# Kernel optimization log

Measured on AMD Instinct MI355X. Metric: run time of the kernel, lower is better.

Reference implementation:

```python
import jax, jax.numpy as jnp
import numpy as np

LN_EPS = 1e-5

def layernorm(x, g, b):
    mu = jnp.mean(x, axis=-1, keepdims=True)
    var = jnp.mean(jnp.square(x - mu), axis=-1, keepdims=True)
    return (x - mu) * jax.lax.rsqrt(var + LN_EPS) * g + b

def setup_inputs() -> dict:
    B, T, C, H = 4, 1024, 1024, 16
    hd = C // H
    key = jax.random.key(0)
    ks = jax.random.split(key, 16)
    s = 0.02
    inp = {
        "x":  jax.random.normal(ks[0], (B, T, C), jnp.float32),
        # per-head QKV projections, stacked over heads: [H, C, hd] / [H, hd]
        "Wq": jax.random.normal(ks[1], (H, C, hd), jnp.float32) * s,
        "bq": jax.random.normal(ks[2], (H, hd), jnp.float32) * s,
        "Wk": jax.random.normal(ks[3], (H, C, hd), jnp.float32) * s,
        "bk": jax.random.normal(ks[4], (H, hd), jnp.float32) * s,
        "Wv": jax.random.normal(ks[5], (H, C, hd), jnp.float32) * s,
        "bv": jax.random.normal(ks[6], (H, hd), jnp.float32) * s,
        # LayerNorm params: ln1, ln2 (decoder), lnf (inside FeedForward)
        "g1": 1.0 + jax.random.normal(ks[7], (C,), jnp.float32) * s,
        "b1": jax.random.normal(ks[8], (C,), jnp.float32) * s,
        "g2": 1.0 + jax.random.normal(ks[9], (C,), jnp.float32) * s,
        "b2": jax.random.normal(ks[10], (C,), jnp.float32) * s,
        "gf": 1.0 + jax.random.normal(ks[11], (C,), jnp.float32) * s,
        "bf": jax.random.normal(ks[12], (C,), jnp.float32) * s,
        # FFN
        "W1": jax.random.normal(ks[13], (C, 4 * C), jnp.float32) * s,
        "b1f": jnp.zeros((4 * C,), jnp.float32),
        "W2": jax.random.normal(ks[14], (4 * C, C), jnp.float32) * s,
        "b2f": jnp.zeros((C,), jnp.float32),
    }
    return inp

def reference(x, Wq, bq, Wk, bk, Wv, bv, g1, b1, g2, b2, gf, bf, W1, b1f, W2, b2f):
    B, T, C = x.shape
    h = layernorm(x, g1, b1)                      # ln1
    # multi-head causal attention (per-head projections stacked on H)
    q = jnp.einsum("btc,hcd->bhtd", h, Wq) + bq[None, :, None, :]
    k = jnp.einsum("btc,hcd->bhtd", h, Wk) + bk[None, :, None, :]
    v = jnp.einsum("btc,hcd->bhtd", h, Wv) + bv[None, :, None, :]
    # NOTE: original scales by C**-0.5 (n_embd), not head_size**-0.5
    att = jnp.einsum("bhtd,bhsd->bhts", q, k) / jnp.sqrt(jnp.float32(C))
    causal = jnp.tril(jnp.ones((T, T), bool))
    att = jnp.where(causal, att, -jnp.inf)
    att = jax.nn.softmax(att, axis=-1)
    o = jnp.einsum("bhts,bhsd->bhtd", att, v)     # [B,H,T,hd]
    o = jnp.transpose(o, (0, 2, 1, 3)).reshape(B, T, C)  # concat heads
    x2 = h + o
    x3 = layernorm(x2, g2, b2)                    # ln2
    # FeedForward: hf = ln(x3); out = net(hf) + hf  (residual uses post-LN!)
    hf = layernorm(x3, gf, bf)
    ff = jax.nn.relu(hf @ W1 + b1f) @ W2 + b2f + hf
    return x3 + ff                                # dropout is identity in eval
```

## Files before the change

### kernel.cpp

```cpp
#include <hip/hip_runtime.h>
#include <hip/hip_bf16.h>


typedef __attribute__((ext_vector_type(8))) short short8;
typedef __attribute__((ext_vector_type(4))) short short4v;
typedef __attribute__((ext_vector_type(4))) float f32x4;

#define DEVI static __device__ __forceinline__

#define BAR() __builtin_amdgcn_s_barrier()
#define SB0() __builtin_amdgcn_sched_barrier(0)
#define LGKM0()                                         \
  {                                                     \
    asm volatile("s_waitcnt lgkmcnt(0)" ::: "memory");  \
    __builtin_amdgcn_sched_barrier(0);                  \
  }
#define VMW(n)                                              \
  {                                                         \
    asm volatile("s_waitcnt vmcnt(" #n ")" ::: "memory");   \
    __builtin_amdgcn_sched_barrier(0);                      \
  }

DEVI void gload_lds16(const void* g, void* l) {
  __builtin_amdgcn_global_load_lds(
      (const __attribute__((address_space(1))) void*)g,
      (__attribute__((address_space(3))) void*)l, 16, 0, 0);
}

DEVI float bf2f(short s) {
  union { float f; unsigned u; } cv;
  cv.u = ((unsigned)(unsigned short)s) << 16;
  return cv.f;
}
DEVI short f2bf(float f) {
  union { float f; unsigned u; } cv;
  cv.f = f;
  unsigned u = cv.u;
  u += 0x7FFFu + ((u >> 16) & 1u);
  return (short)(u >> 16);
}

DEVI void block_reduce2(float& s, float& s2, float* red, int t) {
#pragma unroll
  for (int off = 1; off < 64; off <<= 1) {
    s += __shfl_xor(s, off, 64);
    s2 += __shfl_xor(s2, off, 64);
  }
  __syncthreads();
  if ((t & 63) == 0) { red[(t >> 6) * 2] = s; red[(t >> 6) * 2 + 1] = s2; }
  __syncthreads();
  s = red[0] + red[2] + red[4] + red[6];
  s2 = red[1] + red[3] + red[5] + red[7];
}

DEVI void xcd_swz(int gx, int gy, int& bx, int& by) {
  const int flat = blockIdx.y * gx + blockIdx.x;
  const int c = (gx * gy) >> 3;
  const int nf = (flat & 7) * c + (flat >> 3);
  bx = nf % gx;
  by = nf / gx;
}

__global__ __launch_bounds__(256) void transpose_to_bf16(
    const float* __restrict__ in, short* __restrict__ out, int R, int C) {
  __shared__ float tile[32][33];
  const int b = blockIdx.z;
  in += (size_t)b * R * C;
  out += (size_t)b * R * C;
  const int r0 = blockIdx.y * 32, c0 = blockIdx.x * 32;
  const int tx = threadIdx.x, ty = threadIdx.y;
#pragma unroll
  for (int i = 0; i < 32; i += 8)
    tile[ty + i][tx] = in[(size_t)(r0 + ty + i) * C + c0 + tx];
  __syncthreads();
#pragma unroll
  for (int i = 0; i < 32; i += 8)
    out[(size_t)(c0 + ty + i) * R + r0 + tx] = f2bf(tile[tx][ty + i]);
}

__global__ __launch_bounds__(256) void transpose_qkv(
    const float* __restrict__ Wq, const float* __restrict__ Wk,
    const float* __restrict__ Wv, short* __restrict__ out) {
  __shared__ float tile[32][33];
  const int z = blockIdx.z;
  const int sel = z >> 4, b = z & 15;
  const float* in = (sel == 0) ? Wq : (sel == 1) ? Wk : Wv;
  in += (size_t)b * 1024 * 64;
  short* o = out + (size_t)sel * 1024 * 1024 + (size_t)b * 1024 * 64;
  const int r0 = blockIdx.y * 32, c0 = blockIdx.x * 32;
  const int tx = threadIdx.x, ty = threadIdx.y;
#pragma unroll
  for (int i = 0; i < 32; i += 8)
    tile[ty + i][tx] = in[(size_t)(r0 + ty + i) * 64 + c0 + tx];
  __syncthreads();
#pragma unroll
  for (int i = 0; i < 32; i += 8)
    o[(size_t)(c0 + ty + i) * 1024 + r0 + tx] = f2bf(tile[tx][ty + i]);
}

__global__ __launch_bounds__(256) void ln1_kernel(
    const float* __restrict__ x, const float* __restrict__ g,
    const float* __restrict__ b, short* __restrict__ hb) {
  __shared__ float red[8];
  const int row = blockIdx.x, t = threadIdx.x;
  float4 v = ((const float4*)(x + (size_t)row * 1024))[t];
  float s = v.x + v.y + v.z + v.w;
  float s2 = v.x * v.x + v.y * v.y + v.z * v.z + v.w * v.w;
  block_reduce2(s, s2, red, t);
  const float mu = s * (1.0f / 1024.0f);
  const float rstd = rsqrtf(s2 * (1.0f / 1024.0f) - mu * mu + 1e-5f);
  float4 gv = ((const float4*)g)[t], bv = ((const float4*)b)[t];
  short4v p = {f2bf((v.x - mu) * rstd * gv.x + bv.x),
               f2bf((v.y - mu) * rstd * gv.y + bv.y),
               f2bf((v.z - mu) * rstd * gv.z + bv.z),
               f2bf((v.w - mu) * rstd * gv.w + bv.w)};
  ((short4v*)(hb + (size_t)row * 1024))[t] = p;
}

__global__ __launch_bounds__(256) void ln2f_kernel(
    const short* __restrict__ hbb, const short* __restrict__ ob,
    const float* __restrict__ g2, const float* __restrict__ b2,
    const float* __restrict__ gf, const float* __restrict__ bfp,
    short* __restrict__ x3, short* __restrict__ hfb) {
  __shared__ float red[8];
  const int row = blockIdx.x, t = threadIdx.x;
  short4v hv4 = ((const short4v*)(hbb + (size_t)row * 1024))[t];
  short4v ov4 = ((const short4v*)(ob + (size_t)row * 1024))[t];
  float4 v;
  v.x = bf2f(hv4.x) + bf2f(ov4.x);
  v.y = bf2f(hv4.y) + bf2f(ov4.y);
  v.z = bf2f(hv4.z) + bf2f(ov4.z);
  v.w = bf2f(hv4.w) + bf2f(ov4.w);
  float s = v.x + v.y + v.z + v.w;
  float s2 = v.x * v.x + v.y * v.y + v.z * v.z + v.w * v.w;
  block_reduce2(s, s2, red, t);
  float mu = s * (1.0f / 1024.0f);
  float rstd = rsqrtf(s2 * (1.0f / 1024.0f) - mu * mu + 1e-5f);
  float4 gv = ((const float4*)g2)[t], bv = ((const float4*)b2)[t];
  float4 xv;
  xv.x = (v.x - mu) * rstd * gv.x + bv.x;
  xv.y = (v.y - mu) * rstd * gv.y + bv.y;
  xv.z = (v.z - mu) * rstd * gv.z + bv.z;
  xv.w = (v.w - mu) * rstd * gv.w + bv.w;
  short4v xp = {f2bf(xv.x), f2bf(xv.y), f2bf(xv.z), f2bf(xv.w)};
  ((short4v*)(x3 + (size_t)row * 1024))[t] = xp;
  s = xv.x + xv.y + xv.z + xv.w;
  s2 = xv.x * xv.x + xv.y * xv.y + xv.z * xv.z + xv.w * xv.w;
  block_reduce2(s, s2, red, t);
  mu = s * (1.0f / 1024.0f);
  rstd = rsqrtf(s2 * (1.0f / 1024.0f) - mu * mu + 1e-5f);
  float4 gv2 = ((const float4*)gf)[t], bv2 = ((const float4*)bfp)[t];
  short4v pk = {f2bf((xv.x - mu) * rstd * gv2.x + bv2.x),
                f2bf((xv.y - mu) * rstd * gv2.y + bv2.y),
                f2bf((xv.z - mu) * rstd * gv2.z + bv2.z),
                f2bf((xv.w - mu) * rstd * gv2.w + bv2.w)};
  ((short4v*)(hfb + (size_t)row * 1024))[t] = pk;
}

template <int EPI>
DEVI void gemm8_body(const short* __restrict__ A, const short* __restrict__ B,
                     int K, int kbase, int m0, int n0,
                     const float* __restrict__ f0, const float* __restrict__ f1,
                     const float* __restrict__ f2, short* __restrict__ s0,
                     short* __restrict__ s1, short* __restrict__ s2) {
  extern __shared__ __align__(16) char lds[];
  constexpr int NT = 16;
  const int tid = threadIdx.x;
  const int l = tid & 63, w = tid >> 6;
  const int wrM = w >> 2, wcN = w & 3;
  const int lr = l & 15, lg = l >> 4;

  const int cswz = (((lr & 1) << 2) | lg) ^ (lr >> 1);
  const int laneoff = ((lr >> 1) << 7) + (cswz << 4);

  const int rsel = l >> 3;
  const int scz = (l & 7) ^ rsel;
  const int s_roff = w * 16 + rsel * 2 + (scz >> 2);
  const int s_kc = (scz & 3) * 8;
  const short* Asrc = A + (size_t)(m0 + s_roff) * K + kbase + s_kc;
  const short* Bsrc = B + (size_t)(n0 + s_roff) * K + kbase + s_kc;
  const size_t rstep = (size_t)128 * K;

  auto STAGE = [&](int op, int kh, int t) {
    const short* g = (op ? Bsrc : Asrc) + t * 64 + kh * 32;
    char* d = lds + ((t & 1) * 65536 + op * 32768 + kh * 16384 + w * 1024);
    gload_lds16(g, d);
    gload_lds16(g + rstep, d + 8192);
  };

  f32x4 acc[8][4] = {};

  STAGE(0, 0, 0); STAGE(1, 0, 0); STAGE(0, 1, 0); STAGE(1, 1, 0);
  VMW(4); BAR(); SB0();

  for (int t = 0; t < NT; ++t) {
    const char* pa = lds + (t & 1) * 65536 + wrM * 8192 + laneoff;
    const char* pb = lds + (t & 1) * 65536 + 32768 + wcN * 4096 + laneoff;
    const bool st = (t + 1) < NT;
    short8 a[8], b[4];

#pragma unroll
    for (int mt = 0; mt < 8; ++mt) a[mt] = *(const short8*)(pa + mt * 1024);
#pragma unroll
    for (int nt = 0; nt < 4; ++nt) b[nt] = *(const short8*)(pb + nt * 1024);
    if (st) STAGE(0, 0, t + 1);
    BAR(); LGKM0();
    __builtin_amdgcn_s_setprio(1);
#pragma unroll
    for (int mt = 0; mt < 8; ++mt) {
      acc[mt][0] = __builtin_amdgcn_mfma_f32_16x16x32_bf16(a[mt], b[0], acc[mt][0], 0, 0, 0);
      acc[mt][1] = __builtin_amdgcn_mfma_f32_16x16x32_bf16(a[mt], b[1], acc[mt][1], 0, 0, 0);
    }
    __builtin_amdgcn_s_setprio(0);
    BAR(); SB0();

    if (st) STAGE(1, 0, t + 1);
    BAR(); SB0();
    __builtin_amdgcn_s_setprio(1);
#pragma unroll
    for (int mt = 0; mt < 8; ++mt) {
      acc[mt][2] = __builtin_amdgcn_mfma_f32_16x16x32_bf16(a[mt], b[2], acc[mt][2], 0, 0, 0);
      acc[mt][3] = __builtin_amdgcn_mfma_f32_16x16x32_bf16(a[mt], b[3], acc[mt][3], 0, 0, 0);
    }
    __builtin_amdgcn_s_setprio(0);
    if (st) { VMW(4); } else { VMW(0); }
    BAR(); SB0();

    pa += 16384; pb += 16384;
#pragma unroll
    for (int mt = 0; mt < 8; ++mt) a[mt] = *(const short8*)(pa + mt * 1024);
#pragma unroll
    for (int nt = 0; nt < 4; ++nt) b[nt] = *(const short8*)(pb + nt * 1024);
    if (st) STAGE(0, 1, t + 1);
    BAR(); LGKM0();
    __builtin_amdgcn_s_setprio(1);
#pragma unroll
    for (int mt = 0; mt < 8; ++mt) {
      acc[mt][0] = __builtin_amdgcn_mfma_f32_16x16x32_bf16(a[mt], b[0], acc[mt][0], 0, 0, 0);
      acc[mt][1] = __builtin_amdgcn_mfma_f32_16x16x32_bf16(a[mt], b[1], acc[mt][1], 0, 0, 0);
    }
    __builtin_amdgcn_s_setprio(0);
    BAR(); SB0();

    if (st) STAGE(1, 1, t + 1);
    BAR(); SB0();
    __builtin_amdgcn_s_setprio(1);
#pragma unroll
    for (int mt = 0; mt < 8; ++mt) {
      acc[mt][2] = __builtin_amdgcn_mfma_f32_16x16x32_bf16(a[mt], b[2], acc[mt][2], 0, 0, 0);
      acc[mt][3] = __builtin_amdgcn_mfma_f32_16x16x32_bf16(a[mt], b[3], acc[mt][3], 0, 0, 0);
    }
    __builtin_amdgcn_s_setprio(0);
    if (st) VMW(4);
    BAR(); SB0();
  }

#pragma unroll
  for (int mt = 0; mt < 8; ++mt) {
#pragma unroll
    for (int nt = 0; nt < 4; ++nt) {
      const int col = n0 + wcN * 64 + nt * 16 + lr;
      const int row0 = m0 + wrM * 128 + mt * 16 + lg * 4;
      if constexpr (EPI == 0) {
        const int sel = col >> 10, nn = col & 1023;
        const int hh = nn >> 6, dd = nn & 63;
        const int bb = row0 >> 10, tt0 = row0 & 1023;
        if (sel == 2) {
          const float bias = f2[nn];
          short4v pk = {f2bf(acc[mt][nt][0] + bias), f2bf(acc[mt][nt][1] + bias),
                        f2bf(acc[mt][nt][2] + bias), f2bf(acc[mt][nt][3] + bias)};
          *(short4v*)&s2[(((size_t)(bb * 16 + hh)) * 64 + dd) * 1024 + tt0] = pk;
        } else {
          const float bias = (sel == 0) ? f0[nn] : f1[nn];
          short* dst = (sel == 0) ? s0 : s1;
#pragma unroll
          for (int r = 0; r < 4; ++r)
            dst[(((size_t)(bb * 16 + hh)) * 1024 + tt0 + r) * 64 + dd] =
                f2bf(acc[mt][nt][r] + bias);
        }
      } else if constexpr (EPI == 1) {
#pragma unroll
        for (int r = 0; r < 4; ++r) {
          float val = fmaxf(acc[mt][nt][r] + f0[col], 0.0f);
          s0[(size_t)(row0 + r) * 4096 + col] = f2bf(val);
        }
      } else {
#pragma unroll
        for (int r = 0; r < 4; ++r)
          s0[(size_t)(row0 + r) * 1024 + col] = f2bf(acc[mt][nt][r]);
      }
    }
  }
}

__global__ __launch_bounds__(512, 2) void gemm8_qkv(
    const short* __restrict__ A, const short* __restrict__ B,
    const float* __restrict__ bq, const float* __restrict__ bk,
    const float* __restrict__ bv, short* __restrict__ q,
    short* __restrict__ k, short* __restrict__ vt) {
  int bx, by;
  xcd_swz(12, 16, bx, by);
  gemm8_body<0>(A, B, 1024, 0, by * 256, bx * 256, bq, bk, bv, q, k, vt);
}

__global__ __launch_bounds__(512, 2) void gemm8_ffn1(
    const short* __restrict__ A, const short* __restrict__ B,
    const float* __restrict__ b1f, short* __restrict__ u) {
  int bx, by;
  xcd_swz(16, 16, bx, by);
  gemm8_body<1>(A, B, 1024, 0, by * 256, bx * 256, b1f, nullptr, nullptr, u,
                nullptr, nullptr);
}

__global__ __launch_bounds__(512, 2) void gemm8_ffn2sk(
    const short* __restrict__ A, const short* __restrict__ B,
    short* __restrict__ part) {
  const int z = blockIdx.z;
  int bx, by;
  xcd_swz(4, 16, bx, by);
  gemm8_body<2>(A, B, 4096, z * 1024, by * 256, bx * 256, nullptr, nullptr,
                nullptr, part + (size_t)z * 4096 * 1024, nullptr, nullptr);
}

__global__ __launch_bounds__(256) void ffn2_reduce(
    const short* __restrict__ part, const float* __restrict__ b2f,
    const short* __restrict__ hfb, const short* __restrict__ x3,
    float* __restrict__ out) {
  const size_t i = (size_t)blockIdx.x * 256 + threadIdx.x;
  const size_t S = (size_t)4096 * 1024 / 4;
  short4v a0 = ((const short4v*)part)[i];
  short4v a1 = ((const short4v*)part)[i + S];
  short4v a2 = ((const short4v*)part)[i + 2 * S];
  short4v a3 = ((const short4v*)part)[i + 3 * S];
  float4 bb = ((const float4*)b2f)[i & 255];
  short4v xv = ((const short4v*)x3)[i];
  short4v hv = ((const short4v*)hfb)[i];
  float4 o;
  o.x = bf2f(a0.x) + bf2f(a1.x) + bf2f(a2.x) + bf2f(a3.x) + bb.x + bf2f(hv.x) + bf2f(xv.x);
  o.y = bf2f(a0.y) + bf2f(a1.y) + bf2f(a2.y) + bf2f(a3.y) + bb.y + bf2f(hv.y) + bf2f(xv.y);
  o.z = bf2f(a0.z) + bf2f(a1.z) + bf2f(a2.z) + bf2f(a3.z) + bb.z + bf2f(hv.z) + bf2f(xv.z);
  o.w = bf2f(a0.w) + bf2f(a1.w) + bf2f(a2.w) + bf2f(a3.w) + bb.w + bf2f(hv.w) + bf2f(xv.w);
  ((float4*)out)[i] = o;
}

__global__ __launch_bounds__(256, 5) void attn_kernel(
    const short* __restrict__ q, const short* __restrict__ k,
    const short* __restrict__ vt, short* __restrict__ o) {
  __shared__ __align__(16) short Ksm[64 * 64];
  __shared__ __align__(16) short Vsm[64 * 64];
  __shared__ __align__(16) short Psm[4 * 16 * 64];
  const int bh = blockIdx.x;
  const int qt = 15 - blockIdx.y;
  const int tid = threadIdx.x, lane = tid & 63, w = tid >> 6;
  const int lr = lane & 15, lg = lane >> 4;

  const short* qb = q + (size_t)bh * 1024 * 64;
  const short* kb = k + (size_t)bh * 1024 * 64;
  const short* vb = vt + (size_t)bh * 64 * 1024;

  const int qrow = qt * 64 + w * 16 + lr;
  short8 qf0 = *(const short8*)&qb[(size_t)qrow * 64 + lg * 8];
  short8 qf1 = *(const short8*)&qb[(size_t)qrow * 64 + 32 + lg * 8];

  f32x4 oacc[4] = {};
  float mrun = -1e30f, lrun = 0.0f;

  const float scale2 = 0.03125f * 1.44269504088896f;
  const int srow = tid >> 3;
  const int sc8 = tid & 7;
  char* pw = (char*)(Psm + w * 1024);
  const int qloc = w * 16 + lr;
  const int rowswz = (lr & 7) << 4;

  short8 kreg[2], vreg[2];
#pragma unroll
  for (int p = 0; p < 2; ++p) {
    const int rr = srow + p * 32;
    kreg[p] = *(const short8*)&kb[(size_t)rr * 64 + sc8 * 8];
    vreg[p] = *(const short8*)&vb[(size_t)rr * 1024 + sc8 * 8];
  }

  for (int kt = 0; kt <= qt; ++kt) {
#pragma unroll
    for (int p = 0; p < 2; ++p) {
      const int rr = srow + p * 32;
      *(short8*)((char*)Ksm + rr * 128 + ((sc8 ^ (rr & 7)) << 4)) = kreg[p];
      *(short8*)((char*)Vsm + rr * 128 + ((sc8 ^ (rr & 7)) << 4)) = vreg[p];
    }
    __syncthreads();
    if (kt < qt) {
#pragma unroll
      for (int p = 0; p < 2; ++p) {
        const int rr = srow + p * 32;
        kreg[p] =
            *(const short8*)&kb[((size_t)((kt + 1) * 64 + rr)) * 64 + sc8 * 8];
        vreg[p] =
            *(const short8*)&vb[(size_t)rr * 1024 + (kt + 1) * 64 + sc8 * 8];
      }
    }

    f32x4 sfr[4];
#pragma unroll
    for (int nt = 0; nt < 4; ++nt) {
      const int krow = nt * 16 + lr;
      short8 kf0 = *(const short8*)((const char*)Ksm + krow * 128 +
                                    (((0 + lg) ^ (krow & 7)) << 4));
      short8 kf1 = *(const short8*)((const char*)Ksm + krow * 128 +
                                    (((4 + lg) ^ (krow & 7)) << 4));
      f32x4 z = {};
      z = __builtin_amdgcn_mfma_f32_16x16x32_bf16(kf0, qf0, z, 0, 0, 0);
      z = __builtin_amdgcn_mfma_f32_16x16x32_bf16(kf1, qf1, z, 0, 0, 0);
      sfr[nt] = z;
    }
    if (kt == qt) {
#pragma unroll
      for (int nt = 0; nt < 4; ++nt) {
        const int kb0 = nt * 16 + lg * 4;
#pragma unroll
        for (int r = 0; r < 4; ++r)
          sfr[nt][r] = (kb0 + r <= qloc) ? sfr[nt][r] * scale2 : -1e30f;
      }
    } else {
#pragma unroll
      for (int nt = 0; nt < 4; ++nt)
#pragma unroll
        for (int r = 0; r < 4; ++r) sfr[nt][r] *= scale2;
    }
    float pm;
    {
      float a0 = fmaxf(fmaxf(sfr[0][0], sfr[0][1]), fmaxf(sfr[0][2], sfr[0][3]));
      float a1 = fmaxf(fmaxf(sfr[1][0], sfr[1][1]), fmaxf(sfr[1][2], sfr[1][3]));
      float a2 = fmaxf(fmaxf(sfr[2][0], sfr[2][1]), fmaxf(sfr[2][2], sfr[2][3]));
      float a3 = fmaxf(fmaxf(sfr[3][0], sfr[3][1]), fmaxf(sfr[3][2], sfr[3][3]));
      pm = fmaxf(fmaxf(a0, a1), fmaxf(a2, a3));
      pm = fmaxf(pm, __shfl_xor(pm, 16, 64));
      pm = fmaxf(pm, __shfl_xor(pm, 32, 64));
    }
    if (!__all(pm - mrun <= 8.0f)) {
      const float mnew = fmaxf(mrun, pm);
      const float alpha = exp2f(mrun - mnew);
      mrun = mnew;
      lrun *= alpha;
#pragma unroll
      for (int nt = 0; nt < 4; ++nt)
#pragma unroll
        for (int r = 0; r < 4; ++r) oacc[nt][r] *= alpha;
    }
    float rs;
    {
#pragma unroll
      for (int nt = 0; nt < 4; ++nt)
#pragma unroll
        for (int r = 0; r < 4; ++r) sfr[nt][r] = exp2f(sfr[nt][r] - mrun);
      float s0 = (sfr[0][0] + sfr[0][1]) + (sfr[0][2] + sfr[0][3]);
      float s1 = (sfr[1][0] + sfr[1][1]) + (sfr[1][2] + sfr[1][3]);
      float s2 = (sfr[2][0] + sfr[2][1]) + (sfr[2][2] + sfr[2][3]);
      float s3 = (sfr[3][0] + sfr[3][1]) + (sfr[3][2] + sfr[3][3]);
      rs = (s0 + s1) + (s2 + s3);
      rs += __shfl_xor(rs, 16, 64);
      rs += __shfl_xor(rs, 32, 64);
    }
    lrun += rs;

#pragma unroll
    for (int nt = 0; nt < 4; ++nt) {
      unsigned w0, w1;
      asm("v_cvt_pk_bf16_f32 %0, %1, %2"
          : "=v"(w0) : "v"(sfr[nt][0]), "v"(sfr[nt][1]));
      asm("v_cvt_pk_bf16_f32 %0, %1, %2"
          : "=v"(w1) : "v"(sfr[nt][2]), "v"(sfr[nt][3]));
      uint2 pk2 = {w0, w1};
      *(uint2*)(pw + lr * 128 + ((nt * 32 + lg * 8) ^ rowswz)) = pk2;
    }

#pragma unroll
    for (int kc = 0; kc < 2; ++kc) {
      short8 pb8 = *(const short8*)(pw + lr * 128 + ((kc * 64 + lg * 16) ^ rowswz));
#pragma unroll
      for (int nt = 0; nt < 4; ++nt) {
        const int vrow = nt * 16 + lr;
        short8 vf = *(const short8*)((const char*)Vsm + vrow * 128 +
                                     (((kc * 4 + lg) ^ (vrow & 7)) << 4));
        oacc[nt] = __builtin_amdgcn_mfma_f32_16x16x32_bf16(vf, pb8, oacc[nt], 0, 0, 0);
      }
    }
    __syncthreads();
  }

  const float inv = 1.0f / lrun;
  short* ob = o + (size_t)(bh >> 4) * 1024 * 1024 +
              (size_t)(qt * 64 + qloc) * 1024 + (bh & 15) * 64;
#pragma unroll
  for (int nt = 0; nt < 4; ++nt) {
    short4v pk = {f2bf(oacc[nt][0] * inv), f2bf(oacc[nt][1] * inv),
                  f2bf(oacc[nt][2] * inv), f2bf(oacc[nt][3] * inv)};
    *(short4v*)&ob[nt * 16 + lg * 4] = pk;
  }
}

extern "C" void kernel_launch(void* const* d_in, const int* in_sizes, int n_in,
                              void* d_out, int out_size, void* d_ws,
                              size_t ws_size, hipStream_t stream) {
  const float* x = (const float*)d_in[0];
  const float* Wq = (const float*)d_in[1];
  const float* bq = (const float*)d_in[2];
  const float* Wk = (const float*)d_in[3];
  const float* bk = (const float*)d_in[4];
  const float* Wv = (const float*)d_in[5];
  const float* bv = (const float*)d_in[6];
  const float* g1 = (const float*)d_in[7];
  const float* b1 = (const float*)d_in[8];
  const float* g2 = (const float*)d_in[9];
  const float* b2 = (const float*)d_in[10];
  const float* gf = (const float*)d_in[11];
  const float* bfp = (const float*)d_in[12];
  const float* W1 = (const float*)d_in[13];
  const float* b1f = (const float*)d_in[14];
  const float* W2 = (const float*)d_in[15];
  const float* b2f = (const float*)d_in[16];
  float* out = (float*)d_out;

  hipFuncSetAttribute((const void*)gemm8_qkv,
                      hipFuncAttributeMaxDynamicSharedMemorySize, 131072);
  hipFuncSetAttribute((const void*)gemm8_ffn1,
                      hipFuncAttributeMaxDynamicSharedMemorySize, 131072);
  hipFuncSetAttribute((const void*)gemm8_ffn2sk,
                      hipFuncAttributeMaxDynamicSharedMemorySize, 131072);

  const size_t MB = 1024 * 1024;
  char* p = (char*)d_ws;
  short* qbuf = (short*)(p + 0 * MB);
  short* kbuf = (short*)(p + 8 * MB);
  short* vtb = (short*)(p + 16 * MB);
  short* obuf = (short*)(p + 24 * MB);
  short* wqkv_t = (short*)(p + 32 * MB);
  short* w1_t = (short*)(p + 40 * MB);
  short* part = (short*)(p + 0 * MB);
  char* q = p + 48 * MB;
  short* w2_t = (short*)(q + 0 * MB);
  short* hbb = (short*)(q + 8 * MB);
  short* x3b = (short*)(q + 16 * MB);
  short* hfb = (short*)(q + 24 * MB);
  short* ub = (short*)(q + 32 * MB);

  dim3 tb(32, 8);
  transpose_qkv<<<dim3(2, 32, 48), tb, 0, stream>>>(Wq, Wk, Wv, wqkv_t);
  transpose_to_bf16<<<dim3(128, 32, 1), tb, 0, stream>>>(W1, w1_t, 1024, 4096);
  transpose_to_bf16<<<dim3(32, 128, 1), tb, 0, stream>>>(W2, w2_t, 4096, 1024);

  ln1_kernel<<<4096, 256, 0, stream>>>(x, g1, b1, hbb);

  gemm8_qkv<<<dim3(12, 16), 512, 131072, stream>>>(hbb, wqkv_t, bq, bk, bv,
                                                   qbuf, kbuf, vtb);

  attn_kernel<<<dim3(64, 16), 256, 0, stream>>>(qbuf, kbuf, vtb, obuf);

  ln2f_kernel<<<4096, 256, 0, stream>>>(hbb, obuf, g2, b2, gf, bfp, x3b, hfb);

  gemm8_ffn1<<<dim3(16, 16), 512, 131072, stream>>>(hfb, w1_t, b1f, ub);

  gemm8_ffn2sk<<<dim3(4, 16, 4), 512, 131072, stream>>>(ub, w2_t, part);

  ffn2_reduce<<<4096, 256, 0, stream>>>(part, b2f, hfb, x3b, out);
}
```

Measured before the change: 182.0 us.

## Fuse weight transposes, halve QKV GEMM M-tile, widen FFN2 reduce vectors

Merges the three weight-transpose kernels into one launch that dispatches on block index, which cuts launch overhead. The GEMM body is templated on the M tile size, and the QKV projection uses BM=128 with a 12x32 grid so 384 blocks fill the GPU's CUs more evenly than 192. The final split-K reduce now handles 8 elements per thread with 16-byte loads, using half as many blocks. The smaller QKV tile reduces per-block operand reuse, and the LDS-wait counts are derived from the number of A loads.

```diff
diff --git a/kernel.cpp b/kernel.cpp
--- a/kernel.cpp
+++ b/kernel.cpp
@@ -15,11 +15,12 @@
     asm volatile("s_waitcnt lgkmcnt(0)" ::: "memory");  \
     __builtin_amdgcn_sched_barrier(0);                  \
   }
-#define VMW(n)                                              \
-  {                                                         \
-    asm volatile("s_waitcnt vmcnt(" #n ")" ::: "memory");   \
-    __builtin_amdgcn_sched_barrier(0);                      \
-  }
+
+template <int N>
+DEVI void vmwN() {
+  asm volatile("s_waitcnt vmcnt(%0)" ::"n"(N) : "memory");
+  __builtin_amdgcn_sched_barrier(0);
+}
 
 DEVI void gload_lds16(const void* g, void* l) {
   __builtin_amdgcn_global_load_lds(
@@ -61,41 +62,42 @@
   by = nf / gx;
 }
 
-__global__ __launch_bounds__(256) void transpose_to_bf16(
-    const float* __restrict__ in, short* __restrict__ out, int R, int C) {
+__global__ __launch_bounds__(256) void transpose_all(
+    const float* __restrict__ Wq, const float* __restrict__ Wk,
+    const float* __restrict__ Wv, const float* __restrict__ W1,
+    const float* __restrict__ W2, short* __restrict__ wqkv_t,
+    short* __restrict__ w1_t, short* __restrict__ w2_t) {
   __shared__ float tile[32][33];
-  const int b = blockIdx.z;
-  in += (size_t)b * R * C;
-  out += (size_t)b * R * C;
-  const int r0 = blockIdx.y * 32, c0 = blockIdx.x * 32;
+  const int bid = blockIdx.x;
   const int tx = threadIdx.x, ty = threadIdx.y;
+  const float* in;
+  short* o;
+  int r0, c0, R, C;
+  if (bid < 3072) {
+    const int bx = bid & 1, rem = bid >> 1;
+    const int by = rem & 31, z = rem >> 5;
+    const int sel = z >> 4, b = z & 15;
+    in = ((sel == 0) ? Wq : (sel == 1) ? Wk : Wv) + (size_t)b * 1024 * 64;
+    o = wqkv_t + (size_t)sel * 1024 * 1024 + (size_t)b * 1024 * 64;
+    r0 = by * 32; c0 = bx * 32; R = 1024; C = 64;
+  } else if (bid < 7168) {
+    const int b2 = bid - 3072;
+    const int bx = b2 & 127, by = b2 >> 7;
+    in = W1; o = w1_t;
+    r0 = by * 32; c0 = bx * 32; R = 1024; C = 4096;
+  } else {
+    const int b2 = bid - 7168;
+    const int bx = b2 & 31, by = b2 >> 5;
+    in = W2; o = w2_t;
+    r0 = by * 32; c0 = bx * 32; R = 4096; C = 1024;
+  }
 #pragma unroll
   for (int i = 0; i < 32; i += 8)
     tile[ty + i][tx] = in[(size_t)(r0 + ty + i) * C + c0 + tx];
   __syncthreads();
 #pragma unroll
   for (int i = 0; i < 32; i += 8)
-    out[(size_t)(c0 + ty + i) * R + r0 + tx] = f2bf(tile[tx][ty + i]);
-}
-
-__global__ __launch_bounds__(256) void transpose_qkv(
-    const float* __restrict__ Wq, const float* __restrict__ Wk,
-    const float* __restrict__ Wv, short* __restrict__ out) {
-  __shared__ float tile[32][33];
-  const int z = blockIdx.z;
-  const int sel = z >> 4, b = z & 15;
-  const float* in = (sel == 0) ? Wq : (sel == 1) ? Wk : Wv;
-  in += (size_t)b * 1024 * 64;
-  short* o = out + (size_t)sel * 1024 * 1024 + (size_t)b * 1024 * 64;
-  const int r0 = blockIdx.y * 32, c0 = blockIdx.x * 32;
-  const int tx = threadIdx.x, ty = threadIdx.y;
-#pragma unroll
-  for (int i = 0; i < 32; i += 8)
-    tile[ty + i][tx] = in[(size_t)(r0 + ty + i) * 64 + c0 + tx];
-  __syncthreads();
-#pragma unroll
-  for (int i = 0; i < 32; i += 8)
-    o[(size_t)(c0 + ty + i) * 1024 + r0 + tx] = f2bf(tile[tx][ty + i]);
+    o[(size_t)(c0 + ty + i) * R + r0 + tx] = f2bf(tile[tx][ty + i]);
 }
 
 __global__ __launch_bounds__(256) void ln1_kernel(
@@ -157,7 +159,7 @@
   ((short4v*)(hfb + (size_t)row * 1024))[t] = pk;
 }
 
-template <int EPI>
+template <int EPI, int BM>
 DEVI void gemm8_body(const short* __restrict__ A, const short* __restrict__ B,
                      int K, int kbase, int m0, int n0,
                      const float* __restrict__ f0, const float* __restrict__ f1,
@@ -165,6 +167,11 @@
                      short* __restrict__ s1, short* __restrict__ s2) {
   extern __shared__ __align__(16) char lds[];
   constexpr int NT = 16;
+  constexpr int MT = BM / 32;
+  constexpr int AKH = BM * 64;
+  constexpr int BUFS = 2 * AKH + 32768;
+  constexpr int ALOADS = BM / 128;
+  constexpr int LKH = ALOADS + 2;
   const int tid = threadIdx.x;
   const int l = tid & 63, w = tid >> 6;
   const int wrM = w >> 2, wcN = w & 3;
@@ -181,86 +188,92 @@
   const short* Bsrc = B + (size_t)(n0 + s_roff) * K + kbase + s_kc;
   const size_t rstep = (size_t)128 * K;
 
-  auto STAGE = [&](int op, int kh, int t) {
-    const short* g = (op ? Bsrc : Asrc) + t * 64 + kh * 32;
-    char* d = lds + ((t & 1) * 65536 + op * 32768 + kh * 16384 + w * 1024);
+  auto STAGE_A = [&](int kh, int t) {
+    const short* g = Asrc + t * 64 + kh * 32;
+    char* d = lds + ((t & 1) * BUFS + kh * AKH + w * 1024);
+    gload_lds16(g, d);
+    if constexpr (ALOADS == 2) gload_lds16(g + rstep, d + 8192);
+  };
+  auto STAGE_B = [&](int kh, int t) {
+    const short* g = Bsrc + t * 64 + kh * 32;
+    char* d = lds + ((t & 1) * BUFS + 2 * AKH + kh * 16384 + w * 1024);
     gload_lds16(g, d);
     gload_lds16(g + rstep, d + 8192);
   };
 
-  f32x4 acc[8][4] = {};
-
-  STAGE(0, 0, 0); STAGE(1, 0, 0); STAGE(0, 1, 0); STAGE(1, 1, 0);
-  VMW(4); BAR(); SB0();
+  f32x4 acc[MT][4] = {};
+
+  STAGE_A(0, 0); STAGE_B(0, 0); STAGE_A(1, 0); STAGE_B(1, 0);
+  vmwN<LKH>(); BAR(); SB0();
 
   for (int t = 0; t < NT; ++t) {
-    const char* pa = lds + (t & 1) * 65536 + wrM * 8192 + laneoff;
-    const char* pb = lds + (t & 1) * 65536 + 32768 + wcN * 4096 + laneoff;
+    const char* pa = lds + (t & 1) * BUFS + wrM * (AKH / 2) + laneoff;
+    const char* pb = lds + (t & 1) * BUFS + 2 * AKH + wcN * 4096 + laneoff;
     const bool st = (t + 1) < NT;
-    short8 a[8], b[4];
-
-#pragma unroll
-    for (int mt = 0; mt < 8; ++mt) a[mt] = *(const short8*)(pa + mt * 1024);
+    short8 a[MT], b[4];
+
+#pragma unroll
+    for (int mt = 0; mt < MT; ++mt) a[mt] = *(const short8*)(pa + mt * 1024);
 #pragma unroll
     for (int nt = 0; nt < 4; ++nt) b[nt] = *(const short8*)(pb + nt * 1024);
-    if (st) STAGE(0, 0, t + 1);
+    if (st) STAGE_A(0, t + 1);
     BAR(); LGKM0();
     __builtin_amdgcn_s_setprio(1);
 #pragma unroll
-    for (int mt = 0; mt < 8; ++mt) {
+    for (int mt = 0; mt < MT; ++mt) {
       acc[mt][0] = __builtin_amdgcn_mfma_f32_16x16x32_bf16(a[mt], b[0], acc[mt][0], 0, 0, 0);
       acc[mt][1] = __builtin_amdgcn_mfma_f32_16x16x32_bf16(a[mt], b[1], acc[mt][1], 0, 0, 0);
     }
     __builtin_amdgcn_s_setprio(0);
     BAR(); SB0();
 
-    if (st) STAGE(1, 0, t + 1);
+    if (st) STAGE_B(0, t + 1);
     BAR(); SB0();
     __builtin_amdgcn_s_setprio(1);
 #pragma unroll
-    for (int mt = 0; mt < 8; ++mt) {
+    for (int mt = 0; mt < MT; ++mt) {
       acc[mt][2] = __builtin_amdgcn_mfma_f32_16x16x32_bf16(a[mt], b[2], acc[mt][2], 0, 0, 0);
       acc[mt][3] = __builtin_amdgcn_mfma_f32_16x16x32_bf16(a[mt], b[3], acc[mt][3], 0, 0, 0);
     }
     __builtin_amdgcn_s_setprio(0);
-    if (st) { VMW(4); } else { VMW(0); }
+    if (st) { vmwN<LKH>(); } else { vmwN<0>(); }
     BAR(); SB0();
 
-    pa += 16384; pb += 16384;
-#pragma unroll
-    for (int mt = 0; mt < 8; ++mt) a[mt] = *(const short8*)(pa + mt * 1024);
+    pa += AKH; pb += 16384;
+#pragma unroll
+    for (int mt = 0; mt < MT; ++mt) a[mt] = *(const short8*)(pa + mt * 1024);
 #pragma unroll
     for (int nt = 0; nt < 4; ++nt) b[nt] = *(const short8*)(pb + nt * 1024);
-    if (st) STAGE(0, 1, t + 1);
+    if (st) STAGE_A(1, t + 1);
     BAR(); LGKM0();
     __builtin_amdgcn_s_setprio(1);
 #pragma unroll
-    for (int mt = 0; mt < 8; ++mt) {
+    for (int mt = 0; mt < MT; ++mt) {
       acc[mt][0] = __builtin_amdgcn_mfma_f32_16x16x32_bf16(a[mt], b[0], acc[mt][0], 0, 0, 0);
       acc[mt][1] = __builtin_amdgcn_mfma_f32_16x16x32_bf16(a[mt], b[1], acc[mt][1], 0, 0, 0);
     }
     __builtin_amdgcn_s_setprio(0);
     BAR(); SB0();
 
-    if (st) STAGE(1, 1, t + 1);
+    if (st) STAGE_B(1, t + 1);
     BAR(); SB0();
     __builtin_amdgcn_s_setprio(1);
 #pragma unroll
-    for (int mt = 0; mt < 8; ++mt) {
+    for (int mt = 0; mt < MT; ++mt) {
       acc[mt][2] = __builtin_amdgcn_mfma_f32_16x16x32_bf16(a[mt], b[2], acc[mt][2], 0, 0, 0);
       acc[mt][3] = __builtin_amdgcn_mfma_f32_16x16x32_bf16(a[mt], b[3], acc[mt][3], 0, 0, 0);
     }
     __builtin_amdgcn_s_setprio(0);
-    if (st) VMW(4);
+    if (st) vmwN<LKH>();
     BAR(); SB0();
   }
 
 #pragma unroll
-  for (int mt = 0; mt < 8; ++mt) {
+  for (int mt = 0; mt < MT; ++mt) {
 #pragma unroll
     for (int nt = 0; nt < 4; ++nt) {
       const int col = n0 + wcN * 64 + nt * 16 + lr;
-      const int row0 = m0 + wrM * 128 + mt * 16 + lg * 4;
+      const int row0 = m0 + wrM * (BM / 2) + mt * 16 + lg * 4;
       if constexpr (EPI == 0) {
         const int sel = col >> 10, nn = col & 1023;
         const int hh = nn >> 6, dd = nn & 63;
@@ -299,8 +312,8 @@
     const float* __restrict__ bv, short* __restrict__ q,
     short* __restrict__ k, short* __restrict__ vt) {
   int bx, by;
-  xcd_swz(12, 16, bx, by);
-  gemm8_body<0>(A, B, 1024, 0, by * 256, bx * 256, bq, bk, bv, q, k, vt);
+  xcd_swz(12, 32, bx, by);
+  gemm8_body<0, 128>(A, B, 1024, 0, by * 128, bx * 256, bq, bk, bv, q, k, vt);
 }
 
 __global__ __launch_bounds__(512, 2) void gemm8_ffn1(
@@ -308,8 +321,8 @@
     const float* __restrict__ b1f, short* __restrict__ u) {
   int bx, by;
   xcd_swz(16, 16, bx, by);
-  gemm8_body<1>(A, B, 1024, 0, by * 256, bx * 256, b1f, nullptr, nullptr, u,
-                nullptr, nullptr);
+  gemm8_body<1, 256>(A, B, 1024, 0, by * 256, bx * 256, b1f, nullptr, nullptr,
+                     u, nullptr, nullptr);
 }
 
 __global__ __launch_bounds__(512, 2) void gemm8_ffn2sk(
@@ -318,29 +331,37 @@
   const int z = blockIdx.z;
   int bx, by;
   xcd_swz(4, 16, bx, by);
-  gemm8_body<2>(A, B, 4096, z * 1024, by * 256, bx * 256, nullptr, nullptr,
-                nullptr, part + (size_t)z * 4096 * 1024, nullptr, nullptr);
+  gemm8_body<2, 256>(A, B, 4096, z * 1024, by * 256, bx * 256, nullptr,
+                     nullptr, nullptr, part + (size_t)z * 4096 * 1024, nullptr,
+                     nullptr);
 }
 
 __global__ __launch_bounds__(256) void ffn2_reduce(
     const short* __restrict__ part, const float* __restrict__ b2f,
     const short* __restrict__ hfb, const short* __restrict__ x3,
     float* __restrict__ out) {
-  const size_t i = (size_t)blockIdx.x * 256 + threadIdx.x;
-  const size_t S = (size_t)4096 * 1024 / 4;
-  short4v a0 = ((const short4v*)part)[i];
-  short4v a1 = ((const short4v*)part)[i + S];
-  short4v a2 = ((const short4v*)part)[i + 2 * S];
-  short4v a3 = ((const short4v*)part)[i + 3 * S];
-  float4 bb = ((const float4*)b2f)[i & 255];
-  short4v xv = ((const short4v*)x3)[i];
-  short4v hv = ((const short4v*)hfb)[i];
-  float4 o;
-  o.x = bf2f(a0.x) + bf2f(a1.x) + bf2f(a2.x) + bf2f(a3.x) + bb.x + bf2f(hv.x) + bf2f(xv.x);
-  o.y = bf2f(a0.y) + bf2f(a1.y) + bf2f(a2.y) + bf2f(a3.y) + bb.y + bf2f(hv.y) + bf2f(xv.y);
-  o.z = bf2f(a0.z) + bf2f(a1.z) + bf2f(a2.z) + bf2f(a3.z) + bb.z + bf2f(hv.z) + bf2f(xv.z);
-  o.w = bf2f(a0.w) + bf2f(a1.w) + bf2f(a2.w) + bf2f(a3.w) + bb.w + bf2f(hv.w) + bf2f(xv.w);
-  ((float4*)out)[i] = o;
+  const size_t i8 = (size_t)blockIdx.x * 256 + threadIdx.x;
+  const size_t S = (size_t)4096 * 1024 / 8;
+  short8 a0 = ((const short8*)part)[i8];
+  short8 a1 = ((const short8*)part)[i8 + S];
+  short8 a2 = ((const short8*)part)[i8 + 2 * S];
+  short8 a3 = ((const short8*)part)[i8 + 3 * S];
+  short8 xv = ((const short8*)x3)[i8];
+  short8 hv = ((const short8*)hfb)[i8];
+  const int cb = (int)((i8 * 2) & 255);
+  float4 bb0 = ((const float4*)b2f)[cb];
+  float4 bb1 = ((const float4*)b2f)[cb + 1];
+  float ob[8];
+#pragma unroll
+  for (int j = 0; j < 8; ++j) {
+    const float bbv = j < 4 ? ((const float*)&bb0)[j] : ((const float*)&bb1)[j - 4];
+    ob[j] = bf2f(a0[j]) + bf2f(a1[j]) + bf2f(a2[j]) + bf2f(a3[j]) + bbv +
+            bf2f(hv[j]) + bf2f(xv[j]);
+  }
+  float4 o0 = {ob[0], ob[1], ob[2], ob[3]};
+  float4 o1 = {ob[4], ob[5], ob[6], ob[7]};
+  ((float4*)out)[i8 * 2] = o0;
+  ((float4*)out)[i8 * 2 + 1] = o1;
 }
 
 __global__ __launch_bounds__(256, 5) void attn_kernel(
@@ -520,12 +541,12 @@
   const float* b2f = (const float*)d_in[16];
   float* out = (float*)d_out;
 
-  hipFuncSetAttribute((const void*)gemm8_qkv,
-                      hipFuncAttributeMaxDynamicSharedMemorySize, 131072);
-  hipFuncSetAttribute((const void*)gemm8_ffn1,
-                      hipFuncAttributeMaxDynamicSharedMemorySize, 131072);
-  hipFuncSetAttribute((const void*)gemm8_ffn2sk,
-                      hipFuncAttributeMaxDynamicSharedMemorySize, 131072);
+  (void)hipFuncSetAttribute((const void*)gemm8_qkv,
+                            hipFuncAttributeMaxDynamicSharedMemorySize, 98304);
+  (void)hipFuncSetAttribute((const void*)gemm8_ffn1,
+                            hipFuncAttributeMaxDynamicSharedMemorySize, 131072);
+  (void)hipFuncSetAttribute((const void*)gemm8_ffn2sk,
+                            hipFuncAttributeMaxDynamicSharedMemorySize, 131072);
 
   const size_t MB = 1024 * 1024;
   char* p = (char*)d_ws;
@@ -543,15 +564,13 @@
   short* hfb = (short*)(q + 24 * MB);
   short* ub = (short*)(q + 32 * MB);
 
-  dim3 tb(32, 8);
-  transpose_qkv<<<dim3(2, 32, 48), tb, 0, stream>>>(Wq, Wk, Wv, wqkv_t);
-  transpose_to_bf16<<<dim3(128, 32, 1), tb, 0, stream>>>(W1, w1_t, 1024, 4096);
-  transpose_to_bf16<<<dim3(32, 128, 1), tb, 0, stream>>>(W2, w2_t, 4096, 1024);
+  transpose_all<<<11264, dim3(32, 8), 0, stream>>>(Wq, Wk, Wv, W1, W2, wqkv_t,
+                                                   w1_t, w2_t);
 
   ln1_kernel<<<4096, 256, 0, stream>>>(x, g1, b1, hbb);
 
-  gemm8_qkv<<<dim3(12, 16), 512, 131072, stream>>>(hbb, wqkv_t, bq, bk, bv,
-                                                   qbuf, kbuf, vtb);
+  gemm8_qkv<<<dim3(12, 32), 512, 98304, stream>>>(hbb, wqkv_t, bq, bk, bv,
+                                                  qbuf, kbuf, vtb);
 
   attn_kernel<<<dim3(64, 16), 256, 0, stream>>>(qbuf, kbuf, vtb, obuf);
 
@@ -561,5 +580,5 @@
 
   gemm8_ffn2sk<<<dim3(4, 16, 4), 512, 131072, stream>>>(ub, w2_t, part);
 
-  ffn2_reduce<<<4096, 256, 0, stream>>>(part, b2f, hfb, x3b, out);
-}
+  ffn2_reduce<<<2048, 256, 0, stream>>>(part, b2f, hfb, x3b, out);
+}
```

Result: no change. 181.8 us (-0.1%).
